# Kernel tuning notes

Hardware: AMD Instinct MI355X
Metric: run time of the kernel (lower is better)

Reference implementation:

```python
import jax, jax.numpy as jnp
import numpy as np

EPS = 1e-5
SLOPE = 0.2


def _edge_conv(x, w, gamma, beta, k):
    # x: (B,N,D); w: (O, 2D); returns (B,N,O)
    sq = jnp.sum(x * x, axis=-1)                                  # (B,N)
    # negative squared distance: larger = closer
    neg = 2.0 * jnp.einsum('bnd,bmd->bnm', x, x) - sq[:, :, None] - sq[:, None, :]
    _, idx = jax.lax.top_k(neg, k + 1)                            # (B,N,k+1)
    idx = idx[:, :, 1:]                                           # drop self -> (B,N,k)
    neigh = jax.vmap(lambda xb, ib: xb[ib])(x, idx)               # (B,N,k,D)
    ctr = jnp.broadcast_to(x[:, :, None, :], neigh.shape)
    edge = jnp.concatenate([neigh - ctr, ctr], axis=-1)           # (B,N,k,2D)
    h = jnp.einsum('bnkc,oc->bnko', edge, w)                      # 1x1 conv
    h = h * (gamma / jnp.sqrt(1.0 + EPS)) + beta                  # BN eval (mean=0,var=1)
    h = jnp.where(h > 0, h, SLOPE * h)                            # LeakyReLU(0.2)
    return jnp.max(h, axis=2)                                     # max over k -> (B,N,O)


def _bn_eval(x, gamma, beta):
    return x * (gamma / jnp.sqrt(1.0 + EPS)) + beta


def _lrelu(x):
    return jnp.where(x > 0, x, SLOPE * x)


def setup_inputs() -> dict:
    key = jax.random.key(0)
    ks = jax.random.split(key, 32)
    B, N, D, k, num_classes = 4, 4096, 3, 10, 3
    s = 0.1
    inp = {
        'points': jax.random.normal(ks[0], (B, N, D), jnp.float32),
        'k': k,
        'w1': jax.random.normal(ks[1], (64, 6), jnp.float32) * s,
        'g1': 1.0 + 0.1 * jax.random.normal(ks[2], (64,), jnp.float32),
        'b1': 0.1 * jax.random.normal(ks[3], (64,), jnp.float32),
        'w2': jax.random.normal(ks[4], (64, 128), jnp.float32) * s,
        'g2': 1.0 + 0.1 * jax.random.normal(ks[5], (64,), jnp.float32),
        'b2': 0.1 * jax.random.normal(ks[6], (64,), jnp.float32),
        'w3': jax.random.normal(ks[7], (128, 128), jnp.float32) * s,
        'g3': 1.0 + 0.1 * jax.random.normal(ks[8], (128,), jnp.float32),
        'b3': 0.1 * jax.random.normal(ks[9], (128,), jnp.float32),
        'w4': jax.random.normal(ks[10], (256, 256), jnp.float32) * s,
        'g4': 1.0 + 0.1 * jax.random.normal(ks[11], (256,), jnp.float32),
        'b4': 0.1 * jax.random.normal(ks[12], (256,), jnp.float32),
        'w5': jax.random.normal(ks[13], (1024, 512), jnp.float32) * s,
        'g5': 1.0 + 0.1 * jax.random.normal(ks[14], (1024,), jnp.float32),
        'b5': 0.1 * jax.random.normal(ks[15], (1024,), jnp.float32),
        'fw1': jax.random.normal(ks[16], (512, 1024), jnp.float32) * s,
        'fg1': 1.0 + 0.1 * jax.random.normal(ks[17], (512,), jnp.float32),
        'fbt1': 0.1 * jax.random.normal(ks[18], (512,), jnp.float32),
        'fw2': jax.random.normal(ks[19], (256, 512), jnp.float32) * s,
        'fb2': 0.1 * jax.random.normal(ks[20], (256,), jnp.float32),
        'fg2': 1.0 + 0.1 * jax.random.normal(ks[21], (256,), jnp.float32),
        'fbt2': 0.1 * jax.random.normal(ks[22], (256,), jnp.float32),
        'fw3': jax.random.normal(ks[23], (num_classes, 256), jnp.float32) * s,
        'fb3': 0.1 * jax.random.normal(ks[24], (num_classes,), jnp.float32),
    }
    return inp


def reference(points, w1, g1, b1, w2, g2, b2, w3, g3, b3, w4, g4, b4,
              w5, g5, b5, fw1, fg1, fbt1, fw2, fb2, fg2, fbt2, fw3, fb3, k):
    o1 = _edge_conv(points, w1, g1, b1, k)   # (B,N,64)
    o2 = _edge_conv(o1, w2, g2, b2, k)       # (B,N,64)
    o3 = _edge_conv(o2, w3, g3, b3, k)       # (B,N,128)
    o4 = _edge_conv(o3, w4, g4, b4, k)       # (B,N,256)
    cat = jnp.concatenate([o1, o2, o3, o4], axis=-1)   # (B,N,512)
    h = jnp.einsum('bnc,oc->bno', cat, w5)   # (B,N,1024)
    h = _lrelu(_bn_eval(h, g5, b5))
    h = jnp.max(h, axis=1)                   # global max over N -> (B,1024)
    # fc head (dropout = identity in eval)
    h = _lrelu(_bn_eval(h @ fw1.T, fg1, fbt1))
    h = _lrelu(_bn_eval(h @ fw2.T + fb2, fg2, fbt2))
    out = h @ fw3.T + fb3                    # (B,num_classes)
    return out
```

## Files before the change

### kernel.cpp

```cpp
#include <hip/hip_runtime.h>
#include <math.h>

#define N_PTS 4096
#define BATCH 4
#define KNN 10

__device__ __forceinline__ unsigned f2key(float x) {
    unsigned u = __float_as_uint(x);
    return (u & 0x80000000u) ? ~u : (u | 0x80000000u);
}
__device__ __forceinline__ float key2f(unsigned k) {
    unsigned u = (k & 0x80000000u) ? (k & 0x7FFFFFFFu) : ~k;
    return __uint_as_float(u);
}

__device__ __forceinline__ float lrelu(float h) { return (h > 0.f) ? h : 0.2f * h; }

__device__ __forceinline__ unsigned long long pack_kd(float v, int c) {
    return ((unsigned long long)f2key(v) << 32) | (unsigned)~(unsigned)c;
}

__device__ __forceinline__ unsigned long long bcast64(unsigned long long x, int src) {
    unsigned lo = (unsigned)__builtin_amdgcn_readlane((int)(unsigned)(x & 0xFFFFFFFFu), src);
    unsigned hi = (unsigned)__builtin_amdgcn_readlane((int)(unsigned)(x >> 32), src);
    return ((unsigned long long)hi << 32) | lo;
}

__global__ void sq_kernel(const float* __restrict__ x, int xstr, int D,
                          float* __restrict__ sq) {
    int g = blockIdx.x * blockDim.x + threadIdx.x;
    if (g >= BATCH * N_PTS) return;
    const float* row = x + (long)g * xstr;
    float s = 0.f;
    if ((D & 3) == 0) {
        for (int c = 0; c < D; c += 4) {
            float4 v = *(const float4*)&row[c];
            s += v.x * v.x + v.y * v.y + v.z * v.z + v.w * v.w;
        }
    } else {
        for (int c = 0; c < D; ++c) { float v = row[c]; s += v * v; }
    }
    sq[g] = s;
}

__global__ __launch_bounds__(256) void dist_kernel(const float* __restrict__ x,
                                                   const float* __restrict__ sq,
                                                   float* __restrict__ dist,
                                                   int xstr, int D, int row0) {
    __shared__ float As[16][132];
    __shared__ float Bs[16][132];
    int b = blockIdx.z;
    const float* xb = x + (long)b * N_PTS * xstr;
    const float* sqb = sq + b * N_PTS;
    float* db = dist + (long)b * 1024 * N_PTS;
    int r0 = row0 + blockIdx.y * 128;
    int c0 = blockIdx.x * 128;
    int tx = threadIdx.x & 15, ty = threadIdx.x >> 4;
    float acc[8][8] = {};
    int nk = (D + 15) >> 4;
    for (int kt = 0; kt < nk; ++kt) {
        int k0 = kt * 16;
        for (int e = threadIdx.x; e < 2048; e += 256) {
            int kk = e & 15, r = e >> 4;
            int c = k0 + kk;
            As[kk][r] = (c < D) ? xb[(long)(r0 + r) * xstr + c] : 0.f;
            Bs[kk][r] = (c < D) ? xb[(long)(c0 + r) * xstr + c] : 0.f;
        }
        __syncthreads();
        #pragma unroll
        for (int kk = 0; kk < 16; ++kk) {
            float a[8], bb[8];
            *(float4*)&a[0] = *(float4*)&As[kk][ty * 8];
            *(float4*)&a[4] = *(float4*)&As[kk][ty * 8 + 4];
            *(float4*)&bb[0] = *(float4*)&Bs[kk][tx * 8];
            *(float4*)&bb[4] = *(float4*)&Bs[kk][tx * 8 + 4];
            #pragma unroll
            for (int i = 0; i < 8; ++i)
                #pragma unroll
                for (int j = 0; j < 8; ++j) acc[i][j] += a[i] * bb[j];
        }
        __syncthreads();
    }
    #pragma unroll
    for (int i = 0; i < 8; ++i) {
        int lr = blockIdx.y * 128 + ty * 8 + i;
        float sr = sqb[r0 + ty * 8 + i];
        int cb = c0 + tx * 8;
        float4 v0, v1;
        v0.x = 2.f * acc[i][0] - sr - sqb[cb + 0];
        v0.y = 2.f * acc[i][1] - sr - sqb[cb + 1];
        v0.z = 2.f * acc[i][2] - sr - sqb[cb + 2];
        v0.w = 2.f * acc[i][3] - sr - sqb[cb + 3];
        v1.x = 2.f * acc[i][4] - sr - sqb[cb + 4];
        v1.y = 2.f * acc[i][5] - sr - sqb[cb + 5];
        v1.z = 2.f * acc[i][6] - sr - sqb[cb + 6];
        v1.w = 2.f * acc[i][7] - sr - sqb[cb + 7];
        *(float4*)&db[(long)lr * N_PTS + cb] = v0;
        *(float4*)&db[(long)lr * N_PTS + cb + 4] = v1;
    }
}

__global__ __launch_bounds__(256) void distsym_kernel(const float* __restrict__ x,
                                                      const float* __restrict__ sq,
                                                      float* __restrict__ dist,
                                                      int xstr, int D) {
    __shared__ float As[16][132];
    __shared__ float Bs[16][132];
    __shared__ float Tt[64][132];
    int b = blockIdx.z;
    int t = blockIdx.x, br = 0;
    while (t >= 32 - br) { t -= 32 - br; ++br; }
    int bc = br + t;
    const float* xb = x + (long)b * N_PTS * xstr;
    const float* sqb = sq + b * N_PTS;
    float* db = dist + (long)b * N_PTS * N_PTS;
    int r0 = br * 128, c0 = bc * 128;
    int tx = threadIdx.x & 15, ty = threadIdx.x >> 4;
    float acc[8][8] = {};
    int nk = (D + 15) >> 4;
    for (int kt = 0; kt < nk; ++kt) {
        int k0 = kt * 16;
        for (int e = threadIdx.x; e < 2048; e += 256) {
            int kk = e & 15, r = e >> 4;
            int c = k0 + kk;
            As[kk][r] = (c < D) ? xb[(long)(r0 + r) * xstr + c] : 0.f;
            Bs[kk][r] = (c < D) ? xb[(long)(c0 + r) * xstr + c] : 0.f;
        }
        __syncthreads();
        #pragma unroll
        for (int kk = 0; kk < 16; ++kk) {
            float a[8], bb[8];
            *(float4*)&a[0] = *(float4*)&As[kk][ty * 8];
            *(float4*)&a[4] = *(float4*)&As[kk][ty * 8 + 4];
            *(float4*)&bb[0] = *(float4*)&Bs[kk][tx * 8];
            *(float4*)&bb[4] = *(float4*)&Bs[kk][tx * 8 + 4];
            #pragma unroll
            for (int i = 0; i < 8; ++i)
                #pragma unroll
                for (int j = 0; j < 8; ++j) acc[i][j] += a[i] * bb[j];
        }
        __syncthreads();
    }
    float sqr[8], sqc[8];
    #pragma unroll
    for (int i = 0; i < 8; ++i) sqr[i] = sqb[r0 + ty * 8 + i];
    #pragma unroll
    for (int j = 0; j < 8; ++j) sqc[j] = sqb[c0 + tx * 8 + j];
    #pragma unroll
    for (int i = 0; i < 8; ++i) {
        int R = r0 + ty * 8 + i;
        int cb = c0 + tx * 8;
        float4 v0, v1;
        v0.x = 2.f * acc[i][0] - sqr[i] - sqc[0];
        v0.y = 2.f * acc[i][1] - sqr[i] - sqc[1];
        v0.z = 2.f * acc[i][2] - sqr[i] - sqc[2];
        v0.w = 2.f * acc[i][3] - sqr[i] - sqc[3];
        v1.x = 2.f * acc[i][4] - sqr[i] - sqc[4];
        v1.y = 2.f * acc[i][5] - sqr[i] - sqc[5];
        v1.z = 2.f * acc[i][6] - sqr[i] - sqc[6];
        v1.w = 2.f * acc[i][7] - sqr[i] - sqc[7];
        *(float4*)&db[(long)R * N_PTS + cb] = v0;
        *(float4*)&db[(long)R * N_PTS + cb + 4] = v1;
    }
    if (br == bc) return;
    #pragma unroll
    for (int h = 0; h < 2; ++h) {
        __syncthreads();
        if ((tx >> 3) == h) {
            int txl = tx & 7;
            #pragma unroll
            for (int j = 0; j < 8; ++j)
                #pragma unroll
                for (int i = 0; i < 8; ++i)
                    Tt[txl * 8 + j][ty * 8 + i] =
                        (2.f * acc[i][j] - sqc[j]) - sqr[i];
        }
        __syncthreads();
        for (int e = threadIdx.x; e < 2048; e += 256) {
            int rr = e >> 5, cc = (e & 31) << 2;
            *(float4*)&db[(long)(c0 + h * 64 + rr) * N_PTS + r0 + cc] =
                *(const float4*)&Tt[rr][cc];
        }
    }
}

__global__ __launch_bounds__(256) void topk_kernel(const float* __restrict__ dist,
                                                   int* __restrict__ idxout, int row0) {
    int b = blockIdx.y;
    int wave = threadIdx.x >> 6;
    int lane = threadIdx.x & 63;
    int row_local = blockIdx.x * 4 + wave;
    const float4* d4 =
        (const float4*)(dist + (long)b * 1024 * N_PTS + (long)row_local * N_PTS);

    unsigned long long elem = 0ull;
    unsigned long long T = 0ull;
    float Tf = -INFINITY;

    float4 cur = d4[lane];
    for (int jj = 0; jj < 16; ++jj) {
        float4 nxt;
        if (jj < 15) nxt = d4[(jj + 1) * 64 + lane];
        float vmax = fmaxf(fmaxf(cur.x, cur.y), fmaxf(cur.z, cur.w));
        if (__ballot(vmax >= Tf)) {
            int cbase = jj * 256 + lane * 4;
            unsigned long long kc[4];
            kc[0] = pack_kd(cur.x, cbase + 0);
            kc[1] = pack_kd(cur.y, cbase + 1);
            kc[2] = pack_kd(cur.z, cbase + 2);
            kc[3] = pack_kd(cur.w, cbase + 3);
            #pragma unroll
            for (int q = 0; q < 4; ++q) {
                unsigned long long kq = kc[q];
                unsigned long long mask;
                while ((mask = __ballot(kq > T)) != 0ull) {
                    int src = __ffsll(mask) - 1;
                    unsigned long long kb = bcast64(kq, src);
                    if (lane == src) kq = 0ull;
                    unsigned long long below = __ballot(elem > kb);
                    int pos = __popcll(below);
                    unsigned long long prev = __shfl_up(elem, 1);
                    if (lane == pos) elem = kb;
                    else if (lane > pos && lane <= 10) elem = prev;
                    T = bcast64(elem, 10);
                    Tf = key2f((unsigned)(T >> 32));
                }
            }
        }
        cur = nxt;
    }
    if (lane >= 1 && lane <= 10) {
        int c = (int)~(unsigned)(elem & 0xFFFFFFFFu);
        idxout[((long)b * N_PTS + row0 + row_local) * KNN + (lane - 1)] = c;
    }
}

__global__ __launch_bounds__(256) void topkfull_kernel(const float* __restrict__ dist,
                                                       int* __restrict__ idxout) {
    int b = blockIdx.y;
    int wave = threadIdx.x >> 6;
    int lane = threadIdx.x & 63;
    int row = blockIdx.x * 4 + wave;
    const float4* d4 =
        (const float4*)(dist + (long)b * N_PTS * N_PTS + (long)row * N_PTS);

    unsigned long long elem = 0ull;
    unsigned long long T = 0ull;
    float Tf = -INFINITY;

    float4 buf[4];
    #pragma unroll
    for (int p = 0; p < 4; ++p) buf[p] = d4[p * 64 + lane];
    for (int base = 0; base < 16; base += 4) {
        float4 nbuf[4];
        if (base + 4 < 16) {
            #pragma unroll
            for (int p = 0; p < 4; ++p) nbuf[p] = d4[(base + 4 + p) * 64 + lane];
        }
        #pragma unroll
        for (int p = 0; p < 4; ++p) {
            float4 cur = buf[p];
            float vmax = fmaxf(fmaxf(cur.x, cur.y), fmaxf(cur.z, cur.w));
            if (__ballot(vmax >= Tf)) {
                int cbase = (base + p) * 256 + lane * 4;
                unsigned long long kc[4];
                kc[0] = pack_kd(cur.x, cbase + 0);
                kc[1] = pack_kd(cur.y, cbase + 1);
                kc[2] = pack_kd(cur.z, cbase + 2);
                kc[3] = pack_kd(cur.w, cbase + 3);
                #pragma unroll
                for (int q = 0; q < 4; ++q) {
                    unsigned long long kq = kc[q];
                    unsigned long long mask;
                    while ((mask = __ballot(kq > T)) != 0ull) {
                        int src = __ffsll(mask) - 1;
                        unsigned long long kb = bcast64(kq, src);
                        if (lane == src) kq = 0ull;
                        unsigned long long below = __ballot(elem > kb);
                        int pos = __popcll(below);
                        unsigned long long prev = __shfl_up(elem, 1);
                        if (lane == pos) elem = kb;
                        else if (lane > pos && lane <= 10) elem = prev;
                        T = bcast64(elem, 10);
                        Tf = key2f((unsigned)(T >> 32));
                    }
                }
            }
        }
        #pragma unroll
        for (int p = 0; p < 4; ++p) buf[p] = nbuf[p];
    }
    if (lane >= 1 && lane <= 10) {
        int c = (int)~(unsigned)(elem & 0xFFFFFFFFu);
        idxout[((long)b * N_PTS + row) * KNN + (lane - 1)] = c;
    }
}

template <int DIN, int DOUT, int PTS, int TPP>
__global__ __launch_bounds__(256) void edgeconv_kernel(
    const float* __restrict__ x, int xstr, const int* __restrict__ idx,
    const float* __restrict__ w, const float* __restrict__ gamma,
    const float* __restrict__ beta, float* __restrict__ out, int outoff) {
    constexpr int DP = DIN + 1;
    constexpr int C2 = 2 * DIN;
    __shared__ float ctr[PTS][DP];
    __shared__ float nm[PTS][KNN][DP];
    int p0 = blockIdx.x * PTS;
    for (int e = threadIdx.x; e < PTS * DIN; e += 256) {
        int p = e / DIN, c = e - p * DIN;
        ctr[p][c] = x[(long)(p0 + p) * xstr + c];
    }
    __syncthreads();
    for (int e = threadIdx.x; e < PTS * KNN * DIN; e += 256) {
        int p = e / (KNN * DIN);
        int rem = e - p * (KNN * DIN);
        int kk = rem / DIN, c = rem - kk * DIN;
        int g = p0 + p;
        int nb = (g & ~(N_PTS - 1)) + idx[(long)g * KNN + kk];
        nm[p][kk][c] = x[(long)nb * xstr + c] - ctr[p][c];
    }
    __syncthreads();
    int p = threadIdx.x / TPP;
    int og = (threadIdx.x % TPP) * 4;
    float gs[4], bt[4];
    #pragma unroll
    for (int j = 0; j < 4; ++j) {
        gs[j] = gamma[og + j] / sqrtf(1.f + 1e-5f);
        bt[j] = beta[og + j];
    }
    float base[4] = {0.f, 0.f, 0.f, 0.f};
    for (int c = 0; c < DIN; ++c) {
        float cv = ctr[p][c];
        #pragma unroll
        for (int j = 0; j < 4; ++j) base[j] += cv * w[(og + j) * C2 + DIN + c];
    }
    float acc[KNN][4];
    #pragma unroll
    for (int kk = 0; kk < KNN; ++kk)
        #pragma unroll
        for (int j = 0; j < 4; ++j) acc[kk][j] = base[j];
    for (int c = 0; c < DIN; ++c) {
        float w4[4];
        #pragma unroll
        for (int j = 0; j < 4; ++j) w4[j] = w[(og + j) * C2 + c];
        #pragma unroll
        for (int kk = 0; kk < KNN; ++kk) {
            float nv = nm[p][kk][c];
            #pragma unroll
            for (int j = 0; j < 4; ++j) acc[kk][j] += nv * w4[j];
        }
    }
    float best[4] = {-INFINITY, -INFINITY, -INFINITY, -INFINITY};
    #pragma unroll
    for (int kk = 0; kk < KNN; ++kk)
        #pragma unroll
        for (int j = 0; j < 4; ++j)
            best[j] = fmaxf(best[j], lrelu(acc[kk][j] * gs[j] + bt[j]));
    #pragma unroll
    for (int j = 0; j < 4; ++j)
        out[(long)(p0 + p) * 512 + outoff + og + j] = best[j];
}

template <int DIN, int DOUT>
__global__ __launch_bounds__(256) void uvgemm_kernel(
    const float* __restrict__ x, int xoff, const float* __restrict__ w,
    float* __restrict__ uv) {
    constexpr int NC = 2 * DOUT;
    __shared__ float As[16][132];
    __shared__ float Bs[16][132];
    int r0 = blockIdx.y * 128;
    int c0 = blockIdx.x * 128;
    int tx = threadIdx.x & 15, ty = threadIdx.x >> 4;
    float acc[8][8] = {};
    #pragma unroll 1
    for (int kt = 0; kt < DIN / 16; ++kt) {
        int k0 = kt * 16;
        for (int e = threadIdx.x; e < 2048; e += 256) {
            int kk = e & 15, r = e >> 4;
            As[kk][r] = x[(long)(r0 + r) * 512 + xoff + k0 + kk];
            int jg = c0 + r;
            Bs[kk][r] = (jg < DOUT) ? w[(long)jg * (2 * DIN) + k0 + kk]
                                    : w[(long)(jg - DOUT) * (2 * DIN) + DIN + k0 + kk];
        }
        __syncthreads();
        #pragma unroll
        for (int kk = 0; kk < 16; ++kk) {
            float a[8], bb[8];
            *(float4*)&a[0] = *(float4*)&As[kk][ty * 8];
            *(float4*)&a[4] = *(float4*)&As[kk][ty * 8 + 4];
            *(float4*)&bb[0] = *(float4*)&Bs[kk][tx * 8];
            *(float4*)&bb[4] = *(float4*)&Bs[kk][tx * 8 + 4];
            #pragma unroll
            for (int i = 0; i < 8; ++i)
                #pragma unroll
                for (int j = 0; j < 8; ++j) acc[i][j] += a[i] * bb[j];
        }
        __syncthreads();
    }
    #pragma unroll
    for (int i = 0; i < 8; ++i) {
        int r = r0 + ty * 8 + i;
        int cb = c0 + tx * 8;
        *(float4*)&uv[(long)r * NC + cb] = *(float4*)&acc[i][0];
        *(float4*)&uv[(long)r * NC + cb + 4] = *(float4*)&acc[i][4];
    }
}

template <int DOUT>
__global__ __launch_bounds__(256) void edgemax_kernel(
    const float* __restrict__ uv, const int* __restrict__ idx,
    const float* __restrict__ gamma, const float* __restrict__ beta,
    float* __restrict__ out, int outoff) {
    constexpr int NC = 2 * DOUT;
    constexpr int TPP = DOUT / 4;
    constexpr int TP = 256 / TPP;
    __shared__ int sidx[TP][KNN];
    int p0 = blockIdx.x * TP;
    for (int e = threadIdx.x; e < TP * KNN; e += 256)
        sidx[e / KNN][e % KNN] = idx[(long)(p0 + e / KNN) * KNN + (e % KNN)];
    __syncthreads();
    int p = threadIdx.x / TPP;
    int og = (threadIdx.x % TPP) * 4;
    int g = p0 + p;
    int base_pt = g & ~(N_PTS - 1);
    const float* rowg = uv + (long)g * NC;
    float4 u_n = *(const float4*)&rowg[og];
    float4 v_n = *(const float4*)&rowg[DOUT + og];
    float c0 = v_n.x - u_n.x, c1 = v_n.y - u_n.y;
    float c2 = v_n.z - u_n.z, c3 = v_n.w - u_n.w;
    const float rs = 1.f / sqrtf(1.f + 1e-5f);
    float gs0 = gamma[og + 0] * rs, gs1 = gamma[og + 1] * rs;
    float gs2 = gamma[og + 2] * rs, gs3 = gamma[og + 3] * rs;
    float bt0 = beta[og + 0], bt1 = beta[og + 1];
    float bt2 = beta[og + 2], bt3 = beta[og + 3];
    float b0 = -INFINITY, b1 = -INFINITY, b2 = -INFINITY, b3 = -INFINITY;
    #pragma unroll
    for (int kk = 0; kk < KNN; ++kk) {
        int nb = base_pt + sidx[p][kk];
        float4 ub = *(const float4*)&uv[(long)nb * NC + og];
        b0 = fmaxf(b0, lrelu((ub.x + c0) * gs0 + bt0));
        b1 = fmaxf(b1, lrelu((ub.y + c1) * gs1 + bt1));
        b2 = fmaxf(b2, lrelu((ub.z + c2) * gs2 + bt2));
        b3 = fmaxf(b3, lrelu((ub.w + c3) * gs3 + bt3));
    }
    float4 o4; o4.x = b0; o4.y = b1; o4.z = b2; o4.w = b3;
    *(float4*)&out[(long)g * 512 + outoff + og] = o4;
}

__global__ void init_h5_kernel(unsigned* __restrict__ h5key) {
    int t = blockIdx.x * blockDim.x + threadIdx.x;
    if (t < BATCH * 1024) h5key[t] = 0u;
}

__global__ __launch_bounds__(256) void w5max_kernel(
    const float* __restrict__ cat, const float* __restrict__ w5,
    const float* __restrict__ g5, const float* __restrict__ b5,
    unsigned* __restrict__ h5key) {
    __shared__ float As[16][132];
    __shared__ float Bs[16][132];
    int b = blockIdx.z;
    int n0 = blockIdx.y * 128, o0 = blockIdx.x * 128;
    int tx = threadIdx.x & 15, ty = threadIdx.x >> 4;
    const float* A = cat + (long)b * N_PTS * 512;
    float acc[8][8] = {};
    for (int kt = 0; kt < 32; ++kt) {
        int k0 = kt * 16;
        for (int e = threadIdx.x; e < 2048; e += 256) {
            int kk = e & 15, r = e >> 4;
            As[kk][r] = A[(long)(n0 + r) * 512 + k0 + kk];
            Bs[kk][r] = w5[(long)(o0 + r) * 512 + k0 + kk];
        }
        __syncthreads();
        #pragma unroll
        for (int kk = 0; kk < 16; ++kk) {
            float a[8], bb[8];
            *(float4*)&a[0] = *(float4*)&As[kk][ty * 8];
            *(float4*)&a[4] = *(float4*)&As[kk][ty * 8 + 4];
            *(float4*)&bb[0] = *(float4*)&Bs[kk][tx * 8];
            *(float4*)&bb[4] = *(float4*)&Bs[kk][tx * 8 + 4];
            #pragma unroll
            for (int i = 0; i < 8; ++i)
                #pragma unroll
                for (int j = 0; j < 8; ++j) acc[i][j] += a[i] * bb[j];
        }
        __syncthreads();
    }
    float colmax[8];
    #pragma unroll
    for (int j = 0; j < 8; ++j) {
        int o = o0 + tx * 8 + j;
        float gsc = g5[o] / sqrtf(1.f + 1e-5f);
        float bto = b5[o];
        float m = -INFINITY;
        #pragma unroll
        for (int i = 0; i < 8; ++i)
            m = fmaxf(m, lrelu(acc[i][j] * gsc + bto));
        colmax[j] = m;
    }
    __syncthreads();
    float* red = &As[0][0];
    #pragma unroll
    for (int j = 0; j < 8; ++j) red[ty * 128 + tx * 8 + j] = colmax[j];
    __syncthreads();
    if (threadIdx.x < 128) {
        int col = threadIdx.x;
        float m = -INFINITY;
        #pragma unroll
        for (int t = 0; t < 16; ++t) m = fmaxf(m, red[t * 128 + col]);
        atomicMax(&h5key[b * 1024 + o0 + col], f2key(m));
    }
}

__global__ void fc1_kernel(const unsigned* __restrict__ h5key,
                           const float* __restrict__ fw1,
                           const float* __restrict__ fg1,
                           const float* __restrict__ fbt1,
                           float* __restrict__ f1) {
    int o = blockIdx.x * 256 + threadIdx.x;
    int b = blockIdx.y;
    if (o >= 512) return;
    float s = 0.f;
    for (int c = 0; c < 1024; ++c)
        s += key2f(h5key[b * 1024 + c]) * fw1[o * 1024 + c];
    float h = s * (fg1[o] / sqrtf(1.f + 1e-5f)) + fbt1[o];
    f1[b * 512 + o] = lrelu(h);
}

__global__ void fc2_kernel(const float* __restrict__ f1,
                           const float* __restrict__ fw2,
                           const float* __restrict__ fb2,
                           const float* __restrict__ fg2,
                           const float* __restrict__ fbt2,
                           float* __restrict__ f2) {
    int o = threadIdx.x;
    int b = blockIdx.x;
    float s = fb2[o];
    for (int c = 0; c < 512; ++c) s += f1[b * 512 + c] * fw2[o * 512 + c];
    float h = s * (fg2[o] / sqrtf(1.f + 1e-5f)) + fbt2[o];
    f2[b * 256 + o] = lrelu(h);
}

__global__ void fc3_kernel(const float* __restrict__ f2,
                           const float* __restrict__ fw3,
                           const float* __restrict__ fb3,
                           float* __restrict__ out) {
    int t = threadIdx.x;
    if (t >= BATCH * 3) return;
    int b = t / 3, o = t - b * 3;
    float s = fb3[o];
    for (int c = 0; c < 256; ++c) s += f2[b * 256 + c] * fw3[o * 256 + c];
    out[t] = s;
}

extern "C" void kernel_launch(void* const* d_in, const int* in_sizes, int n_in,
                              void* d_out, int out_size, void* d_ws, size_t ws_size,
                              hipStream_t stream) {
    const float* points = (const float*)d_in[0];
    const float* w1 = (const float*)d_in[2];
    const float* g1 = (const float*)d_in[3];
    const float* b1 = (const float*)d_in[4];
    const float* w2 = (const float*)d_in[5];
    const float* g2 = (const float*)d_in[6];
    const float* b2 = (const float*)d_in[7];
    const float* w3 = (const float*)d_in[8];
    const float* g3 = (const float*)d_in[9];
    const float* b3 = (const float*)d_in[10];
    const float* w4 = (const float*)d_in[11];
    const float* g4 = (const float*)d_in[12];
    const float* b4 = (const float*)d_in[13];
    const float* w5 = (const float*)d_in[14];
    const float* g5 = (const float*)d_in[15];
    const float* b5 = (const float*)d_in[16];
    const float* fw1 = (const float*)d_in[17];
    const float* fg1 = (const float*)d_in[18];
    const float* fbt1 = (const float*)d_in[19];
    const float* fw2 = (const float*)d_in[20];
    const float* fb2 = (const float*)d_in[21];
    const float* fg2 = (const float*)d_in[22];
    const float* fbt2 = (const float*)d_in[23];
    const float* fw3 = (const float*)d_in[24];
    const float* fb3 = (const float*)d_in[25];

    float* ws = (float*)d_ws;
    float* cat = ws;
    float* sq = cat + (long)BATCH * N_PTS * 512;
    unsigned* h5key = (unsigned*)(sq + BATCH * N_PTS);
    float* f1 = (float*)(h5key + BATCH * 1024);
    float* f2 = f1 + BATCH * 512;
    int* idxbuf = (int*)(f2 + BATCH * 256);
    float* dist = (float*)(idxbuf + (long)BATCH * N_PTS * KNN);
    float* uv = dist;

    size_t need = (size_t)((char*)(dist + (size_t)BATCH * N_PTS * N_PTS) -
                           (char*)d_ws);
    bool fullp = ws_size >= need;

    auto knn = [&](const float* xbase, int xstr, int D) {
        sq_kernel<<<64, 256, 0, stream>>>(xbase, xstr, D, sq);
        if (fullp) {
            distsym_kernel<<<dim3(528, 1, BATCH), 256, 0, stream>>>(
                xbase, sq, dist, xstr, D);
            topkfull_kernel<<<dim3(N_PTS / 4, BATCH), 256, 0, stream>>>(dist, idxbuf);
        } else {
            for (int r0 = 0; r0 < N_PTS; r0 += 1024) {
                dist_kernel<<<dim3(32, 8, BATCH), 256, 0, stream>>>(xbase, sq, dist,
                                                                    xstr, D, r0);
                topk_kernel<<<dim3(256, BATCH), 256, 0, stream>>>(dist, idxbuf, r0);
            }
        }
    };

    knn(points, 3, 3);
    edgeconv_kernel<3, 64, 16, 16><<<N_PTS * BATCH / 16, 256, 0, stream>>>(
        points, 3, idxbuf, w1, g1, b1, cat, 0);

    knn(cat + 0, 512, 64);
    uvgemm_kernel<64, 64><<<dim3(1, 128), 256, 0, stream>>>(cat, 0, w2, uv);
    edgemax_kernel<64><<<1024, 256, 0, stream>>>(uv, idxbuf, g2, b2, cat, 64);

    knn(cat + 64, 512, 64);
    uvgemm_kernel<64, 128><<<dim3(2, 128), 256, 0, stream>>>(cat, 64, w3, uv);
    edgemax_kernel<128><<<2048, 256, 0, stream>>>(uv, idxbuf, g3, b3, cat, 128);

    knn(cat + 128, 512, 128);
    uvgemm_kernel<128, 256><<<dim3(4, 128), 256, 0, stream>>>(cat, 128, w4, uv);
    edgemax_kernel<256><<<4096, 256, 0, stream>>>(uv, idxbuf, g4, b4, cat, 256);

    init_h5_kernel<<<16, 256, 0, stream>>>(h5key);
    w5max_kernel<<<dim3(8, 32, BATCH), 256, 0, stream>>>(cat, w5, g5, b5, h5key);

    fc1_kernel<<<dim3(2, BATCH), 256, 0, stream>>>(h5key, fw1, fg1, fbt1, f1);
    fc2_kernel<<<BATCH, 256, 0, stream>>>(f1, fw2, fb2, fg2, fbt2, f2);
    fc3_kernel<<<1, 64, 0, stream>>>(f2, fw3, fb3, (float*)d_out);
}
```

Before: 1.783 ms.

## Fuse first-layer distance and top-k into streaming kNN kernel; merge FC head

For the 3-D input layer, a new kernel computes distances on the fly, one wave per query row, and keeps a running sorted top-11 list in registers using ballots and shuffles. This replaces the full distance matrix write plus a separate top-k pass. The three FC-head kernels are also merged into one per-batch kernel that stages intermediates in shared memory, saving two launches. The streaming kNN uses a serial insertion loop that may be costly early on, and it relies on ties being broken consistently by the packed index.

Result: faster. 1.734 ms (-2.7%).

```diff
diff --git a/kernel.cpp b/kernel.cpp
--- a/kernel.cpp
+++ b/kernel.cpp
@@ -41,6 +41,58 @@
         for (int c = 0; c < D; ++c) { float v = row[c]; s += v * v; }
     }
     sq[g] = s;
+}
+
+__global__ __launch_bounds__(256) void knn3_kernel(const float* __restrict__ x,
+                                                   const float* __restrict__ sq,
+                                                   int* __restrict__ idxout) {
+    int b = blockIdx.y;
+    int wave = threadIdx.x >> 6;
+    int lane = threadIdx.x & 63;
+    int row = blockIdx.x * 4 + wave;
+    const float* xb = x + (long)b * N_PTS * 3;
+    const float* sqb = sq + b * N_PTS;
+    float x0 = xb[row * 3 + 0], x1 = xb[row * 3 + 1], x2 = xb[row * 3 + 2];
+    float sr = sqb[row];
+
+    unsigned long long elem = 0ull, T = 0ull;
+    float Tf = -INFINITY;
+
+    int c = lane;
+    float y0 = xb[c * 3 + 0], y1 = xb[c * 3 + 1], y2 = xb[c * 3 + 2];
+    float sc = sqb[c];
+    for (int it = 0; it < 64; ++it) {
+        float ny0, ny1, ny2, nsc;
+        int nc = c + 64;
+        if (it < 63) {
+            ny0 = xb[nc * 3 + 0]; ny1 = xb[nc * 3 + 1]; ny2 = xb[nc * 3 + 2];
+            nsc = sqb[nc];
+        }
+        float s = 0.f;
+        s += x0 * y0; s += x1 * y1; s += x2 * y2;
+        float d = 2.f * s - sr - sc;
+        if (__ballot(d >= Tf)) {
+            unsigned long long kq = pack_kd(d, c);
+            unsigned long long mask;
+            while ((mask = __ballot(kq > T)) != 0ull) {
+                int src = __ffsll(mask) - 1;
+                unsigned long long kb = bcast64(kq, src);
+                if (lane == src) kq = 0ull;
+                unsigned long long below = __ballot(elem > kb);
+                int pos = __popcll(below);
+                unsigned long long prev = __shfl_up(elem, 1);
+                if (lane == pos) elem = kb;
+                else if (lane > pos && lane <= 10) elem = prev;
+                T = bcast64(elem, 10);
+                Tf = key2f((unsigned)(T >> 32));
+            }
+        }
+        y0 = ny0; y1 = ny1; y2 = ny2; sc = nsc; c = nc;
+    }
+    if (lane >= 1 && lane <= 10) {
+        idxout[((long)b * N_PTS + row) * KNN + (lane - 1)] =
+            (int)~(unsigned)(elem & 0xFFFFFFFFull);
+    }
 }
 
 __global__ __launch_bounds__(256) void dist_kernel(const float* __restrict__ x,
@@ -511,45 +563,42 @@
     }
 }
 
-__global__ void fc1_kernel(const unsigned* __restrict__ h5key,
-                           const float* __restrict__ fw1,
-                           const float* __restrict__ fg1,
-                           const float* __restrict__ fbt1,
-                           float* __restrict__ f1) {
-    int o = blockIdx.x * 256 + threadIdx.x;
-    int b = blockIdx.y;
-    if (o >= 512) return;
-    float s = 0.f;
-    for (int c = 0; c < 1024; ++c)
-        s += key2f(h5key[b * 1024 + c]) * fw1[o * 1024 + c];
-    float h = s * (fg1[o] / sqrtf(1.f + 1e-5f)) + fbt1[o];
-    f1[b * 512 + o] = lrelu(h);
-}
-
-__global__ void fc2_kernel(const float* __restrict__ f1,
-                           const float* __restrict__ fw2,
-                           const float* __restrict__ fb2,
-                           const float* __restrict__ fg2,
-                           const float* __restrict__ fbt2,
-                           float* __restrict__ f2) {
-    int o = threadIdx.x;
+__global__ __launch_bounds__(256) void fchead_kernel(
+    const unsigned* __restrict__ h5key,
+    const float* __restrict__ fw1, const float* __restrict__ fg1,
+    const float* __restrict__ fbt1,
+    const float* __restrict__ fw2, const float* __restrict__ fb2,
+    const float* __restrict__ fg2, const float* __restrict__ fbt2,
+    const float* __restrict__ fw3, const float* __restrict__ fb3,
+    float* __restrict__ out) {
+    __shared__ float h5[1024];
+    __shared__ float f1s[512];
+    __shared__ float f2s[256];
     int b = blockIdx.x;
-    float s = fb2[o];
-    for (int c = 0; c < 512; ++c) s += f1[b * 512 + c] * fw2[o * 512 + c];
-    float h = s * (fg2[o] / sqrtf(1.f + 1e-5f)) + fbt2[o];
-    f2[b * 256 + o] = lrelu(h);
-}
-
-__global__ void fc3_kernel(const float* __restrict__ f2,
-                           const float* __restrict__ fw3,
-                           const float* __restrict__ fb3,
-                           float* __restrict__ out) {
-    int t = threadIdx.x;
-    if (t >= BATCH * 3) return;
-    int b = t / 3, o = t - b * 3;
-    float s = fb3[o];
-    for (int c = 0; c < 256; ++c) s += f2[b * 256 + c] * fw3[o * 256 + c];
-    out[t] = s;
+    int tid = threadIdx.x;
+    for (int i = tid; i < 1024; i += 256) h5[i] = key2f(h5key[b * 1024 + i]);
+    __syncthreads();
+    for (int o = tid; o < 512; o += 256) {
+        float s = 0.f;
+        for (int c = 0; c < 1024; ++c) s += h5[c] * fw1[o * 1024 + c];
+        float h = s * (fg1[o] / sqrtf(1.f + 1e-5f)) + fbt1[o];
+        f1s[o] = lrelu(h);
+    }
+    __syncthreads();
+    {
+        int o = tid;
+        float s = fb2[o];
+        for (int c = 0; c < 512; ++c) s += f1s[c] * fw2[o * 512 + c];
+        float h = s * (fg2[o] / sqrtf(1.f + 1e-5f)) + fbt2[o];
+        f2s[o] = lrelu(h);
+    }
+    __syncthreads();
+    if (tid < 3) {
+        int o = tid;
+        float s = fb3[o];
+        for (int c = 0; c < 256; ++c) s += f2s[c] * fw3[o * 256 + c];
+        out[b * 3 + o] = s;
+    }
 }
 
 extern "C" void kernel_launch(void* const* d_in, const int* in_sizes, int n_in,
@@ -610,7 +659,8 @@
         }
     };
 
-    knn(points, 3, 3);
+    sq_kernel<<<64, 256, 0, stream>>>(points, 3, 3, sq);
+    knn3_kernel<<<dim3(N_PTS / 4, BATCH), 256, 0, stream>>>(points, sq, idxbuf);
     edgeconv_kernel<3, 64, 16, 16><<<N_PTS * BATCH / 16, 256, 0, stream>>>(
         points, 3, idxbuf, w1, g1, b1, cat, 0);
 
@@ -629,7 +679,6 @@
     init_h5_kernel<<<16, 256, 0, stream>>>(h5key);
     w5max_kernel<<<dim3(8, 32, BATCH), 256, 0, stream>>>(cat, w5, g5, b5, h5key);
 
-    fc1_kernel<<<dim3(2, BATCH), 256, 0, stream>>>(h5key, fw1, fg1, fbt1, f1);
-    fc2_kernel<<<BATCH, 256, 0, stream>>>(f1, fw2, fb2, fg2, fbt2, f2);
-    fc3_kernel<<<1, 64, 0, stream>>>(f2, fw3, fb3, (float*)d_out);
-}
+    fchead_kernel<<<BATCH, 256, 0, stream>>>(h5key, fw1, fg1, fbt1, fw2, fb2,
+                                             fg2, fbt2, fw3, fb3, (float*)d_out);
+}
```
